# Kernel optimization log

Hardware: AMD Instinct MI355X
Metric: run time of the kernel (lower is better)

Reference implementation:

```python
import jax, jax.numpy as jnp
import numpy as np

B, N, K, CIN, COUT = 2, 8192, 16, 64, 64


def setup_inputs() -> dict:
    key = jax.random.key(0)
    ks = jax.random.split(key, 12)
    w = lambda k, shape: jax.random.normal(k, shape, jnp.float32) * 0.02
    return dict(
        pos=jax.random.normal(ks[0], (B, N, 3), jnp.float32),
        features=jax.random.normal(ks[1], (B, N, CIN), jnp.float32),
        emb_w=w(ks[2], (CIN, COUT)), emb_b=jnp.zeros((COUT,), jnp.float32),
        wq=w(ks[3], (COUT, COUT)), wk=w(ks[4], (COUT, COUT)), wv=w(ks[5], (COUT, COUT)),
        pe_w1=w(ks[6], (3, COUT)), pe_b1=jnp.zeros((COUT,), jnp.float32),
        pe_w2=w(ks[7], (COUT, COUT)), pe_b2=jnp.zeros((COUT,), jnp.float32),
        at_w1=w(ks[8], (COUT, COUT)), at_b1=jnp.zeros((COUT,), jnp.float32),
        at_w2=w(ks[9], (COUT, COUT)), at_b2=jnp.zeros((COUT,), jnp.float32),
        out_w=w(ks[10], (COUT, CIN)), out_b=jnp.zeros((CIN,), jnp.float32),
    )


def _gather(x, idx):
    # x: [B, N, C], idx: [B, N, K] -> [B, N, K, C]
    return jax.vmap(lambda xb, ib: xb[ib])(x, idx)


def reference(pos, features, emb_w, emb_b, wq, wk, wv,
              pe_w1, pe_b1, pe_w2, pe_b2,
              at_w1, at_b1, at_w2, at_b2, out_w, out_b):
    # KNN: squared pairwise distances, take k smallest (includes self)
    sq = jnp.sum(pos * pos, axis=-1)                                  # [B, N]
    d2 = sq[:, :, None] + sq[:, None, :] - 2.0 * jnp.einsum('bnd,bmd->bnm', pos, pos)
    _, knn_idx = jax.lax.top_k(-d2, K)                                # [B, N, K]

    # recenter_groups: neighbor positions relative to query point
    grouped_pos = _gather(pos, knn_idx) - pos[:, :, None, :]          # [B, N, K, 3]

    x = features @ emb_w + emb_b                                      # [B, N, COUT]
    q = x @ wq                                                        # [B, N, COUT]
    k = _gather(x @ wk, knn_idx)                                      # [B, N, K, COUT]
    v = _gather(x @ wv, knn_idx)                                      # [B, N, K, COUT]

    # mlp_posenc: Linear(3,C) -> ReLU -> Linear(C,C)
    posenc = jax.nn.relu(grouped_pos @ pe_w1 + pe_b1) @ pe_w2 + pe_b2  # [B, N, K, COUT]

    # mlp_attn on (q - k + posenc), softmax over neighbor axis (dim=-2)
    h = q[:, :, None, :] - k + posenc
    attn = jax.nn.relu(h @ at_w1 + at_b1) @ at_w2 + at_b2
    attn = jax.nn.softmax(attn / np.float32(np.sqrt(COUT)), axis=-2)

    result = jnp.einsum('bmnf,bmnf->bmf', attn, v + posenc)           # [B, N, COUT]
    return result @ out_w + out_b + features                          # [B, N, CIN]
```

## Files before the change

kernel.cpp:

```cpp
#include <hip/hip_runtime.h>
#include <hip/hip_bf16.h>

#define BB 2
#define NN 8192
#define SPL 16
#define CAND (NN/SPL)
#define NPTS (BB*NN)

#define POS4_OFF 0u
#define PART_OFF 65536u
#define IDX_OFF  4259840u
#define WT_OFF   4521984u
#define QB_OFF   4530176u
#define KVB_OFF  5578752u

typedef __attribute__((ext_vector_type(8))) short bf16x8;
typedef __attribute__((ext_vector_type(4))) float f32x4;

__device__ __forceinline__ unsigned umn(unsigned a, unsigned b) {
#if __has_builtin(__builtin_elementwise_min)
  return __builtin_elementwise_min(a, b);
#else
  return a < b ? a : b;
#endif
}
__device__ __forceinline__ unsigned umx(unsigned a, unsigned b) {
#if __has_builtin(__builtin_elementwise_max)
  return __builtin_elementwise_max(a, b);
#else
  return a < b ? b : a;
#endif
}

__device__ inline unsigned short f2bf(float x) {
  __hip_bfloat16 b = __float2bfloat16(x);
  return *(unsigned short*)&b;
}

#define HCOL(c, j) ((((((c) >> 3) + (j)) & 7) << 3) | ((c) & 7))

__global__ __launch_bounds__(256) void s1_stage(
    const float* __restrict__ pos,
    const float* __restrict__ pe_w2, const float* __restrict__ at_w1,
    const float* __restrict__ at_w2, const float* __restrict__ out_w,
    float* __restrict__ ws)
{
  const int t = blockIdx.x * 256 + threadIdx.x;
  if (t < NPTS) {
    float x = pos[t * 3 + 0], y = pos[t * 3 + 1], z = pos[t * 3 + 2];
    float* o = ws + POS4_OFF + t * 4;
    o[0] = x; o[1] = y; o[2] = z;
    o[3] = fmaf(x, x, fmaf(y, y, z * z));
    return;
  }
  const int u = t - NPTS;
  const float* s;
  switch (u >> 12) {
    case 0: s = pe_w2; break;
    case 1: s = at_w1; break;
    case 2: s = at_w2; break;
    default: s = out_w; break;
  }
  const int idx = u & 4095, f = idx >> 6, c = idx & 63;
  ((unsigned short*)(ws + WT_OFF))[u] = f2bf(s[c * 64 + f]);
}

__global__ __launch_bounds__(256) void s2_knn_qkv(
    const float* __restrict__ feat,
    const float* __restrict__ emb_w, const float* __restrict__ emb_b,
    const float* __restrict__ wq, const float* __restrict__ wk,
    const float* __restrict__ wv,
    float* __restrict__ ws)
{
  __shared__ __align__(16) float smem[6144];
  const int tid = threadIdx.x;
  const int bx = blockIdx.x;
  const float* pos4 = ws + POS4_OFF;
  unsigned* part = (unsigned*)ws + PART_OFF;
  float* qg = ws + QB_OFF;
  unsigned* kvp = (unsigned*)ws + KVB_OFF;

  if (bx < 1024) {
    constexpr int OE[63][2] = {
      {0,1},{2,3},{4,5},{6,7},{8,9},{10,11},{12,13},{14,15},
      {0,2},{1,3},{4,6},{5,7},{8,10},{9,11},{12,14},{13,15},
      {1,2},{5,6},{9,10},{13,14},
      {0,4},{1,5},{2,6},{3,7},{8,12},{9,13},{10,14},{11,15},
      {2,4},{3,5},{10,12},{11,13},
      {1,2},{3,4},{5,6},{9,10},{11,12},{13,14},
      {0,8},{1,9},{2,10},{3,11},{4,12},{5,13},{6,14},{7,15},
      {4,8},{5,9},{6,10},{7,11},
      {2,4},{3,5},{6,8},{7,9},{10,12},{11,13},
      {1,2},{3,4},{5,6},{7,8},{9,10},{11,12},{13,14}
    };
    const int g = (bx & 63) * 256 + tid;
    const int s = bx >> 6;
    const int bu = __builtin_amdgcn_readfirstlane(g >> 13);
    const float4* allp = (const float4*)pos4;
    const float4 q = allp[g];
    const float qx2 = -2.f * q.x, qy2 = -2.f * q.y, qz2 = -2.f * q.z;
    const float sqq = q.w + 1e-5f;
    const float4* cand = allp + (bu * NN + s * CAND);
    const unsigned jb = (unsigned)(s * CAND);
    unsigned m[16];
#pragma unroll
    for (int i = 0; i < 16; i++) m[i] = 0xFFFFFFFFu;
    for (int j0 = 0; j0 < CAND; j0 += 16) {
      unsigned b[16];
#pragma unroll
      for (int i = 0; i < 16; i++) {
        float4 cp = cand[j0 + i];
        float d2 = fmaf(cp.x, qx2, fmaf(cp.y, qy2, fmaf(cp.z, qz2, cp.w + sqq)));
        b[i] = (__float_as_uint(d2) & 0xFFFFE000u) | (jb + (unsigned)(j0 + i));
      }
#pragma unroll
      for (int cc = 0; cc < 63; cc++) {
        const int x = OE[cc][0], y = OE[cc][1];
        unsigned lo = umn(b[x], b[y]);
        unsigned hi = umx(b[x], b[y]);
        b[x] = hi; b[y] = lo;
      }
#pragma unroll
      for (int i = 0; i < 16; i++) m[i] = umn(m[i], b[i]);
#pragma unroll
      for (int d = 8; d; d >>= 1) {
#pragma unroll
        for (int i = 0; i < 16; i++) {
          if ((i & d) == 0) {
            const int l = i | d;
            unsigned lo = umn(m[i], m[l]);
            unsigned hi = umx(m[i], m[l]);
            m[i] = lo; m[l] = hi;
          }
        }
      }
    }
#pragma unroll
    for (int i = 0; i < 16; i++)
      part[(unsigned)(s * 16 + i) * NPTS + (unsigned)g] = m[i];
  } else {
    float* wl = smem;
    float* xl = smem + 4096;
    const int vb = bx - 1024;
    const int col = tid & 63;
    const int rg = tid >> 6;
    const int row0 = vb * 32 + rg * 8;
    const int rowu = __builtin_amdgcn_readfirstlane(row0);
    for (int i = tid; i < 4096; i += 256) wl[i] = emb_w[i];
    __syncthreads();
    {
      float acc[8];
      float bias = emb_b[col];
#pragma unroll
      for (int r = 0; r < 8; r++) acc[r] = bias;
      for (int c = 0; c < 64; c++) {
        float w = wl[c * 64 + col];
        const float* fp = feat + rowu * 64 + c;
#pragma unroll
        for (int r = 0; r < 8; r++) acc[r] = fmaf(fp[r * 64], w, acc[r]);
      }
#pragma unroll
      for (int r = 0; r < 8; r++) xl[(rg * 8 + r) * 64 + col] = acc[r];
    }
    __syncthreads();
    for (int i = tid; i < 4096; i += 256) wl[i] = wq[i];
    __syncthreads();
    {
      float aq[8];
#pragma unroll
      for (int r = 0; r < 8; r++) aq[r] = 0.f;
      for (int c = 0; c < 64; c++) {
        float w = wl[c * 64 + col];
#pragma unroll
        for (int r = 0; r < 8; r++)
          aq[r] = fmaf(xl[(rg * 8 + r) * 64 + c], w, aq[r]);
      }
#pragma unroll
      for (int r = 0; r < 8; r++) qg[(row0 + r) * 64 + col] = aq[r];
    }
    __syncthreads();
    for (int i = tid; i < 4096; i += 256) wl[i] = wk[i];
    __syncthreads();
    float ak[8];
    {
#pragma unroll
      for (int r = 0; r < 8; r++) ak[r] = 0.f;
      for (int c = 0; c < 64; c++) {
        float w = wl[c * 64 + col];
#pragma unroll
        for (int r = 0; r < 8; r++)
          ak[r] = fmaf(xl[(rg * 8 + r) * 64 + c], w, ak[r]);
      }
    }
    __syncthreads();
    for (int i = tid; i < 4096; i += 256) wl[i] = wv[i];
    __syncthreads();
    {
      float av[8];
#pragma unroll
      for (int r = 0; r < 8; r++) av[r] = 0.f;
      for (int c = 0; c < 64; c++) {
        float w = wl[c * 64 + col];
#pragma unroll
        for (int r = 0; r < 8; r++)
          av[r] = fmaf(xl[(rg * 8 + r) * 64 + c], w, av[r]);
      }
#pragma unroll
      for (int r = 0; r < 8; r++)
        kvp[(row0 + r) * 64 + col] =
            ((unsigned)f2bf(av[r]) << 16) | (unsigned)f2bf(ak[r]);
    }
  }
}

__global__ __launch_bounds__(256) void s3_merge(const float* __restrict__ ws_ro,
                                                int* __restrict__ knn_idx)
{
  const unsigned* part = (const unsigned*)ws_ro + PART_OFF;
  const int g = blockIdx.x * 256 + threadIdx.x;
  unsigned run[16];
#pragma unroll
  for (int i = 0; i < 16; i++) run[i] = part[i * NPTS + g];
#pragma unroll
  for (int l = 1; l < SPL; l++) {
#pragma unroll
    for (int i = 0; i < 16; i++)
      run[i] = umn(run[i], part[(l * 16 + 15 - i) * NPTS + g]);
#pragma unroll
    for (int d = 8; d; d >>= 1) {
#pragma unroll
      for (int i = 0; i < 16; i++) {
        if ((i & d) == 0) {
          const int l2 = i | d;
          unsigned lo = umn(run[i], run[l2]);
          unsigned hi = umx(run[i], run[l2]);
          run[i] = lo; run[l2] = hi;
        }
      }
    }
  }
  const int base = (g >> 13) * NN;
  int outv[16];
#pragma unroll
  for (int i = 0; i < 16; i++) outv[i] = base + (int)(run[i] & 0x1FFFu);
  int4* o = (int4*)(knn_idx + g * 16);
  o[0] = make_int4(outv[0], outv[1], outv[2], outv[3]);
  o[1] = make_int4(outv[4], outv[5], outv[6], outv[7]);
  o[2] = make_int4(outv[8], outv[9], outv[10], outv[11]);
  o[3] = make_int4(outv[12], outv[13], outv[14], outv[15]);
}

__device__ inline void mv(const unsigned short* hm, const bf16x8 B[4][2],
                          const float bias[4], int ln, int s0, int s1,
                          f32x4 acc[4])
{
  bf16x8 a0 = *(const bf16x8*)(hm + ln * 64 + s0);
  bf16x8 a1 = *(const bf16x8*)(hm + ln * 64 + s1);
#pragma unroll
  for (int t = 0; t < 4; t++) {
    f32x4 a = {bias[t], bias[t], bias[t], bias[t]};
    a = __builtin_amdgcn_mfma_f32_16x16x32_bf16(a0, B[t][0], a, 0, 0, 0);
    a = __builtin_amdgcn_mfma_f32_16x16x32_bf16(a1, B[t][1], a, 0, 0, 0);
    acc[t] = a;
  }
}

__global__ __launch_bounds__(256, 2) void s4_attn(
    const float* __restrict__ ws_ro, const float* __restrict__ feat,
    const float* __restrict__ pe_w1, const float* __restrict__ pe_b1,
    const float* __restrict__ pe_b2, const float* __restrict__ at_b1,
    const float* __restrict__ at_b2, const float* __restrict__ out_b,
    const int* __restrict__ knn, float* __restrict__ out)
{
  __shared__ unsigned short hma[4][1024];
  __shared__ unsigned short resm[1024];
  const float* pos4 = ws_ro + POS4_OFF;
  const float* qg = ws_ro + QB_OFF;
  const unsigned* kvp = (const unsigned*)ws_ro + KVB_OFF;
  const unsigned short* wt = (const unsigned short*)(ws_ro + WT_OFF);

  const int tid = threadIdx.x;
  const int wid = tid >> 6, lane = tid & 63;
  const int ln = lane & 15, quad = lane >> 4;
  unsigned short* hm = hma[wid];
  const int s0 = ((quad + ln) & 7) << 3;
  const int s1 = ((4 + quad + ln) & 7) << 3;

  bf16x8 Bf[3][4][2];
#pragma unroll
  for (int m = 0; m < 3; m++)
#pragma unroll
    for (int t = 0; t < 4; t++)
#pragma unroll
      for (int ks = 0; ks < 2; ks++)
        Bf[m][t][ks] = *(const bf16x8*)(wt + m * 4096 + (t * 16 + ln) * 64 +
                                        ks * 32 + quad * 8);
  bf16x8 bo[2];
#pragma unroll
  for (int ks = 0; ks < 2; ks++)
    bo[ks] = *(const bf16x8*)(wt + 3 * 4096 + (wid * 16 + ln) * 64 +
                              ks * 32 + quad * 8);

  float pw10 = pe_w1[lane], pw11 = pe_w1[64 + lane], pw12 = pe_w1[128 + lane];
  float pb1 = pe_b1[lane];
  float bpe[4], ba1[4], ba2[4];
#pragma unroll
  for (int t = 0; t < 4; t++) {
    bpe[t] = pe_b2[t * 16 + ln];
    ba1[t] = at_b1[t * 16 + ln];
    ba2[t] = at_b2[t * 16 + ln];
  }
  const float4* pp4 = (const float4*)pos4;

  const int p0 = blockIdx.x * 16 + wid * 4;
  const int ps0 = __builtin_amdgcn_readfirstlane(p0);
  int4 cur[4];
  {
    const int4* ip4 = (const int4*)(knn + ps0 * 16);
#pragma unroll
    for (int u = 0; u < 4; u++) cur[u] = ip4[u];
  }

  for (int pp = 0; pp < 4; pp++) {
    const int p = p0 + pp;
    const int ps = __builtin_amdgcn_readfirstlane(p);
    int jj[16];
#pragma unroll
    for (int u = 0; u < 4; u++) {
      jj[u*4+0] = cur[u].x; jj[u*4+1] = cur[u].y;
      jj[u*4+2] = cur[u].z; jj[u*4+3] = cur[u].w;
    }
    int4 nxt[4];
    {
      const int pn = (pp < 3) ? (ps + 1) : ps;
      const int4* np4 = (const int4*)(knn + pn * 16);
#pragma unroll
      for (int u = 0; u < 4; u++) nxt[u] = np4[u];
    }
    unsigned kvw[4][4];
#pragma unroll
    for (int r = 0; r < 4; r++) {
      const unsigned* kp = kvp + jj[quad * 4 + r] * 64 + ln;
#pragma unroll
      for (int t = 0; t < 4; t++) kvw[r][t] = kp[t * 16];
    }
    float qv[4];
#pragma unroll
    for (int t = 0; t < 4; t++) qv[t] = qg[p * 64 + t * 16 + ln];

    const float4 mp = pp4[ps];
#pragma unroll
    for (int j = 0; j < 16; j++) {
      const float4 np = pp4[jj[j]];
      float h1 = fmaf(np.z - mp.z, pw12,
                 fmaf(np.y - mp.y, pw11,
                 fmaf(np.x - mp.x, pw10, pb1)));
      hm[j * 64 + HCOL(lane, j)] = f2bf(fmaxf(h1, 0.f));
    }
    f32x4 accp[4];
    mv(hm, Bf[0], bpe, ln, s0, s1, accp);
    float vpe[4][4];
#pragma unroll
    for (int r = 0; r < 4; r++) {
      const int j = quad * 4 + r;
#pragma unroll
      for (int t = 0; t < 4; t++) {
        const unsigned w = kvw[r][t];
        float kf = __uint_as_float(w << 16);
        float vf = __uint_as_float(w & 0xFFFF0000u);
        float pe = accp[t][r];
        vpe[t][r] = vf + pe;
        hm[j * 64 + HCOL(t * 16 + ln, j)] = f2bf(qv[t] - kf + pe);
      }
    }
    f32x4 acch[4];
    mv(hm, Bf[1], ba1, ln, s0, s1, acch);
#pragma unroll
    for (int t = 0; t < 4; t++)
#pragma unroll
      for (int r = 0; r < 4; r++) {
        const int j = quad * 4 + r;
        hm[j * 64 + HCOL(t * 16 + ln, j)] = f2bf(fmaxf(acch[t][r], 0.f));
      }
    f32x4 lg[4];
    mv(hm, Bf[2], ba2, ln, s0, s1, lg);
    const int pb = wid * 4 + pp;
#pragma unroll
    for (int t = 0; t < 4; t++) {
      float e0 = __expf(lg[t][0] * 0.125f);
      float e1 = __expf(lg[t][1] * 0.125f);
      float e2 = __expf(lg[t][2] * 0.125f);
      float e3 = __expf(lg[t][3] * 0.125f);
      float ss = (e0 + e1) + (e2 + e3);
      float dt = fmaf(e3, vpe[t][3], fmaf(e2, vpe[t][2],
                 fmaf(e1, vpe[t][1], e0 * vpe[t][0])));
      ss += __shfl_xor(ss, 16); ss += __shfl_xor(ss, 32);
      dt += __shfl_xor(dt, 16); dt += __shfl_xor(dt, 32);
      float res = dt / ss;
      if (quad == 0) resm[pb * 64 + HCOL(t * 16 + ln, pb)] = f2bf(res);
    }
#pragma unroll
    for (int u = 0; u < 4; u++) cur[u] = nxt[u];
  }
  __syncthreads();
  {
    const int nt = wid;
    float ob = out_b[nt * 16 + ln];
    f32x4 acc = {ob, ob, ob, ob};
#pragma unroll
    for (int ks = 0; ks < 2; ks++) {
      bf16x8 a = *(const bf16x8*)(resm + ln * 64 +
                                  (((ks * 4 + quad + ln) & 7) << 3));
      acc = __builtin_amdgcn_mfma_f32_16x16x32_bf16(a, bo[ks], acc, 0, 0, 0);
    }
#pragma unroll
    for (int r = 0; r < 4; r++) {
      const int pt = blockIdx.x * 16 + quad * 4 + r;
      const int f = nt * 16 + ln;
      out[pt * 64 + f] = acc[r] + feat[pt * 64 + f];
    }
  }
}

extern "C" void kernel_launch(void* const* d_in, const int* in_sizes, int n_in,
                              void* d_out, int out_size, void* d_ws, size_t ws_size,
                              hipStream_t stream)
{
  (void)in_sizes; (void)n_in; (void)out_size; (void)ws_size;
  const float* pos   = (const float*)d_in[0];
  const float* feat  = (const float*)d_in[1];
  const float* emb_w = (const float*)d_in[2];
  const float* emb_b = (const float*)d_in[3];
  const float* wq    = (const float*)d_in[4];
  const float* wk    = (const float*)d_in[5];
  const float* wv    = (const float*)d_in[6];
  const float* pe_w1 = (const float*)d_in[7];
  const float* pe_b1 = (const float*)d_in[8];
  const float* pe_w2 = (const float*)d_in[9];
  const float* pe_b2 = (const float*)d_in[10];
  const float* at_w1 = (const float*)d_in[11];
  const float* at_b1 = (const float*)d_in[12];
  const float* at_w2 = (const float*)d_in[13];
  const float* at_b2 = (const float*)d_in[14];
  const float* out_w = (const float*)d_in[15];
  const float* out_b = (const float*)d_in[16];
  float* ws = (float*)d_ws;

  s1_stage<<<128, 256, 0, stream>>>(pos, pe_w2, at_w1, at_w2, out_w, ws);
  s2_knn_qkv<<<1536, 256, 0, stream>>>(feat, emb_w, emb_b, wq, wk, wv, ws);
  s3_merge<<<64, 256, 0, stream>>>(ws, (int*)ws + IDX_OFF);
  s4_attn<<<NPTS / 16, 256, 0, stream>>>(ws, feat, pe_w1, pe_b1, pe_b2,
      at_b1, at_b2, out_b, (int*)ws + IDX_OFF, (float*)d_out);
}
```

Baseline: 228.4 us.

## Merge staging kernel into KNN/QKV kernel and compute distances from raw positions

Removes the separate staging launch. KNN blocks now read the raw xyz positions directly and compute distance as a difference of coordinates instead of the expanded form over precomputed float4 positions. The QKV blocks write padded positions for later stages, and extra blocks convert the weights to bf16. This saves a launch and the dependency between the two kernels, but KNN now does scalar unaligned 3-float loads and a few more ALU ops per candidate.

```diff
diff --git a/kernel.cpp b/kernel.cpp
--- a/kernel.cpp
+++ b/kernel.cpp
@@ -39,43 +39,19 @@
 
 #define HCOL(c, j) ((((((c) >> 3) + (j)) & 7) << 3) | ((c) & 7))
 
-__global__ __launch_bounds__(256) void s1_stage(
-    const float* __restrict__ pos,
-    const float* __restrict__ pe_w2, const float* __restrict__ at_w1,
-    const float* __restrict__ at_w2, const float* __restrict__ out_w,
-    float* __restrict__ ws)
-{
-  const int t = blockIdx.x * 256 + threadIdx.x;
-  if (t < NPTS) {
-    float x = pos[t * 3 + 0], y = pos[t * 3 + 1], z = pos[t * 3 + 2];
-    float* o = ws + POS4_OFF + t * 4;
-    o[0] = x; o[1] = y; o[2] = z;
-    o[3] = fmaf(x, x, fmaf(y, y, z * z));
-    return;
-  }
-  const int u = t - NPTS;
-  const float* s;
-  switch (u >> 12) {
-    case 0: s = pe_w2; break;
-    case 1: s = at_w1; break;
-    case 2: s = at_w2; break;
-    default: s = out_w; break;
-  }
-  const int idx = u & 4095, f = idx >> 6, c = idx & 63;
-  ((unsigned short*)(ws + WT_OFF))[u] = f2bf(s[c * 64 + f]);
-}
-
-__global__ __launch_bounds__(256) void s2_knn_qkv(
-    const float* __restrict__ feat,
+__global__ __launch_bounds__(256) void mega1(
+    const float* __restrict__ pos, const float* __restrict__ feat,
     const float* __restrict__ emb_w, const float* __restrict__ emb_b,
     const float* __restrict__ wq, const float* __restrict__ wk,
     const float* __restrict__ wv,
+    const float* __restrict__ pe_w2, const float* __restrict__ at_w1,
+    const float* __restrict__ at_w2, const float* __restrict__ out_w,
     float* __restrict__ ws)
 {
   __shared__ __align__(16) float smem[6144];
   const int tid = threadIdx.x;
   const int bx = blockIdx.x;
-  const float* pos4 = ws + POS4_OFF;
+  float* pos4 = ws + POS4_OFF;
   unsigned* part = (unsigned*)ws + PART_OFF;
   float* qg = ws + QB_OFF;
   unsigned* kvp = (unsigned*)ws + KVB_OFF;
@@ -96,21 +72,23 @@
     const int g = (bx & 63) * 256 + tid;
     const int s = bx >> 6;
     const int bu = __builtin_amdgcn_readfirstlane(g >> 13);
-    const float4* allp = (const float4*)pos4;
-    const float4 q = allp[g];
-    const float qx2 = -2.f * q.x, qy2 = -2.f * q.y, qz2 = -2.f * q.z;
-    const float sqq = q.w + 1e-5f;
-    const float4* cand = allp + (bu * NN + s * CAND);
+    const float qx = pos[g * 3 + 0], qy = pos[g * 3 + 1], qz = pos[g * 3 + 2];
+    const float* __restrict__ cp = pos + (bu * NN + s * CAND) * 3;
     const unsigned jb = (unsigned)(s * CAND);
     unsigned m[16];
 #pragma unroll
     for (int i = 0; i < 16; i++) m[i] = 0xFFFFFFFFu;
     for (int j0 = 0; j0 < CAND; j0 += 16) {
+      float c[48];
+#pragma unroll
+      for (int i = 0; i < 48; i++) c[i] = cp[j0 * 3 + i];
       unsigned b[16];
 #pragma unroll
       for (int i = 0; i < 16; i++) {
-        float4 cp = cand[j0 + i];
-        float d2 = fmaf(cp.x, qx2, fmaf(cp.y, qy2, fmaf(cp.z, qz2, cp.w + sqq)));
+        float dx = c[i * 3 + 0] - qx;
+        float dy = c[i * 3 + 1] - qy;
+        float dz = c[i * 3 + 2] - qz;
+        float d2 = fmaf(dx, dx, fmaf(dy, dy, dz * dz));
         b[i] = (__float_as_uint(d2) & 0xFFFFE000u) | (jb + (unsigned)(j0 + i));
       }
 #pragma unroll
@@ -138,7 +116,7 @@
 #pragma unroll
     for (int i = 0; i < 16; i++)
       part[(unsigned)(s * 16 + i) * NPTS + (unsigned)g] = m[i];
-  } else {
+  } else if (bx < 1536) {
     float* wl = smem;
     float* xl = smem + 4096;
     const int vb = bx - 1024;
@@ -146,6 +124,12 @@
     const int rg = tid >> 6;
     const int row0 = vb * 32 + rg * 8;
     const int rowu = __builtin_amdgcn_readfirstlane(row0);
+    if (tid < 32) {
+      const int p = vb * 32 + tid;
+      float x = pos[p * 3 + 0], y = pos[p * 3 + 1], z = pos[p * 3 + 2];
+      float4 v = {x, y, z, 0.f};
+      ((float4*)pos4)[p] = v;
+    }
     for (int i = tid; i < 4096; i += 256) wl[i] = emb_w[i];
     __syncthreads();
     {
@@ -210,6 +194,17 @@
         kvp[(row0 + r) * 64 + col] =
             ((unsigned)f2bf(av[r]) << 16) | (unsigned)f2bf(ak[r]);
     }
+  } else {
+    const int t = (bx - 1536) * 256 + tid;
+    const float* s;
+    switch (t >> 12) {
+      case 0: s = pe_w2; break;
+      case 1: s = at_w1; break;
+      case 2: s = at_w2; break;
+      default: s = out_w; break;
+    }
+    const int idx = t & 4095, f = idx >> 6, c = idx & 63;
+    ((unsigned short*)(ws + WT_OFF))[t] = f2bf(s[c * 64 + f]);
   }
 }
 
@@ -446,8 +441,8 @@
   const float* out_b = (const float*)d_in[16];
   float* ws = (float*)d_ws;
 
-  s1_stage<<<128, 256, 0, stream>>>(pos, pe_w2, at_w1, at_w2, out_w, ws);
-  s2_knn_qkv<<<1536, 256, 0, stream>>>(feat, emb_w, emb_b, wq, wk, wv, ws);
+  mega1<<<1600, 256, 0, stream>>>(pos, feat, emb_w, emb_b, wq, wk, wv,
+                                  pe_w2, at_w1, at_w2, out_w, ws);
   s3_merge<<<64, 256, 0, stream>>>(ws, (int*)ws + IDX_OFF);
   s4_attn<<<NPTS / 16, 256, 0, stream>>>(ws, feat, pe_w1, pe_b1, pe_b2,
       at_b1, at_b2, out_b, (int*)ws + IDX_OFF, (float*)d_out);
```

Result: no change. 224.2 us (-1.8%).
